# Optimization experiments

Measured on AMD Instinct MI355X. Metric: run time of the kernel, lower is better.

The kernel has to match this reference:

```python
import jax, jax.numpy as jnp
import numpy as np

BATCH, T, C = 32, 600, 64
DEPTH = 2            # logsig depth 2 -> [increments, Levy areas]
N_SEGMENTS = 50
N_HIDDENS = 512
LOGSIG_CH = C + C * (C - 1) // 2   # 2080, Lyndon-word count at depth 2
IN_SIZE = C + LOGSIG_CH            # 2144 = logsig + start point


def _t_vec(nT, n_segments):
    # matches: [int(round(x)) for x in np.linspace(1, nT, n_segments+1)]
    return np.asarray([int(round(v)) for v in np.linspace(1, nT, n_segments + 1)])


def setup_inputs() -> dict:
    key = jax.random.key(0)
    k0, k1, k2, k3, k4 = jax.random.split(key, 5)
    x = jax.random.normal(k0, (BATCH, T, C), jnp.float32)
    s = 1.0 / np.sqrt(N_HIDDENS)
    w_ih = jax.random.uniform(k1, (4 * N_HIDDENS, IN_SIZE), jnp.float32, -s, s)
    w_hh = jax.random.uniform(k2, (4 * N_HIDDENS, N_HIDDENS), jnp.float32, -s, s)
    b_ih = jax.random.uniform(k3, (4 * N_HIDDENS,), jnp.float32, -s, s)
    b_hh = jax.random.uniform(k4, (4 * N_HIDDENS,), jnp.float32, -s, s)
    return {"x": x, "w_ih": w_ih, "w_hh": w_hh, "b_ih": b_ih, "b_hh": b_hh}


def _logsig_and_start(x):
    """Depth-2 segmented log-signature + segment start points.
    Returns (logsig (B,S,LOGSIG_CH), start (B,S,C))."""
    B, nT, c = x.shape
    tv = _t_vec(nT, N_SEGMENTS)
    starts = tv[:-1] - 1               # segment start frame indices
    ends = tv[1:] - 1                  # segment end frame indices
    # step s (between frames s and s+1) belongs to segment i iff tv[i]-1 <= s < tv[i+1]-1
    step_ids = jnp.asarray(np.searchsorted(tv[1:] - 1, np.arange(nT - 1), side='right'))
    dx = x[:, 1:] - x[:, :-1]                            # (B, T-1, C)
    # per-step outer product x_{t-} (X) dx_t, then segmented sum over steps
    prod = jnp.einsum('btc,btd->btcd', x[:, :-1], dx)    # (B, T-1, C, C)
    Q = jax.ops.segment_sum(jnp.moveaxis(prod, 1, 0), step_ids,
                            num_segments=N_SEGMENTS)      # (S, B, C, C)
    xa = x[:, starts]                                    # (B, S, C)
    xb = x[:, ends]
    inc = xb - xa                                        # level-1 logsig
    # shift origin to segment start: P = sum (X_rel (X) dX)
    P = jnp.moveaxis(Q, 0, 1) - jnp.einsum('bsc,bsd->bscd', xa, inc)
    A = 0.5 * (P - jnp.swapaxes(P, -1, -2))              # Levy area (antisym)
    iu, ju = np.triu_indices(c, 1)                       # Lyndon words (i,j), i<j, lex order
    logsig = jnp.concatenate([inc, A[:, :, iu, ju]], axis=-1)
    return logsig, xa


def _lstm(feats, w_ih, w_hh, b_ih, b_hh):
    B = feats.shape[0]
    H = N_HIDDENS
    gx = jnp.einsum('bsf,gf->bsg', feats, w_ih) + b_ih + b_hh  # (B,S,4H)

    def step(carry, g_t):
        h, cc = carry
        g = g_t + h @ w_hh.T
        i, f, gg, o = jnp.split(g, 4, axis=-1)
        i = jax.nn.sigmoid(i); f = jax.nn.sigmoid(f)
        gg = jnp.tanh(gg); o = jax.nn.sigmoid(o)
        cc = f * cc + i * gg
        h = o * jnp.tanh(cc)
        return (h, cc), h

    h0 = jnp.zeros((B, H), feats.dtype)
    (_, _), hs = jax.lax.scan(step, (h0, h0), jnp.moveaxis(gx, 1, 0))
    return jnp.moveaxis(hs, 0, 1)                        # (B, S, H)


def reference(x, w_ih, w_hh, b_ih, b_hh):
    logsig, x_sp = _logsig_and_start(x)
    feats = jnp.concatenate([logsig, x_sp], axis=-1)      # (B, S, IN_SIZE)
    return _lstm(feats, w_ih, w_hh, b_ih, b_hh)
```

## Files before the change

kernel.cpp:

```cpp
#include <hip/hip_runtime.h>
#include <math.h>

typedef _Float16 f16;
typedef _Float16 f16x8 __attribute__((ext_vector_type(8)));
typedef _Float16 f16x4 __attribute__((ext_vector_type(4)));
typedef float    f32x4 __attribute__((ext_vector_type(4)));

#define BATCH 32
#define TT    600
#define CC    64
#define SEG   50
#define HH    512
#define G4    2048
#define FF    2144
#define MM    1600
#define MP    1664
#define NPAIR 2016
#define CVB   512
#define WRK   208
#define SLOT16 16384

struct TV { int v[51]; };

__device__ __forceinline__ void async_copy16(char* lds, const char* g) {
  __builtin_amdgcn_global_load_lds(
      (const __attribute__((address_space(1))) unsigned int*)g,
      (__attribute__((address_space(3))) unsigned int*)lds, 16, 0, 0);
}

__device__ __forceinline__ float sigm(float x) { return 1.f / (1.f + __expf(-x)); }
__device__ __forceinline__ float tanh_(float x) {
  float ax = fabsf(x);
  float e  = __expf(2.f * ax);
  float t  = 1.f - 2.f / (e + 1.f);
  return x < 0.f ? -t : t;
}
__device__ __forceinline__ unsigned short f16_bits(f16 v) {
  union { f16 f; unsigned short u; } c; c.f = v; return c.u;
}
__device__ __forceinline__ unsigned int f32_bits(float v) {
  union { float f; unsigned int u; } c; c.f = v; return c.u;
}

__global__ void prep_kernel(const float* __restrict__ x, f16* __restrict__ fhi, TV tv,
                            const float4* __restrict__ w_ih, const float4* __restrict__ w_hh,
                            f16x4* __restrict__ w16, f16x4* __restrict__ whh16,
                            unsigned int* __restrict__ ready) {
  __shared__ float xs[13 * CC];
  int m   = blockIdx.x;
  int tid = threadIdx.x;

  if (m >= MP) {
    int cb   = m - MP;
    int gtid = cb * 256 + tid;
    int nth  = CVB * 256;
    for (int i = gtid; i < G4 * FF / 4; i += nth) {
      float4 v = w_ih[i];
      f16x4 o = {(f16)v.x, (f16)v.y, (f16)v.z, (f16)v.w};
      w16[i] = o;
    }
    for (int i = gtid; i < G4 * HH / 4; i += nth) {
      float4 v = w_hh[i];
      f16x4 o = {(f16)v.x, (f16)v.y, (f16)v.z, (f16)v.w};
      whh16[i] = o;
    }
    if (cb == 0)
      for (int i = tid; i < 544; i += 256) ready[i] = 0u;
    return;
  }

  f16* rhi = fhi + (size_t)m * FF;
  if (m >= MM) {
    unsigned int* a = (unsigned int*)rhi;
    for (int i = tid; i < FF / 2; i += 256) a[i] = 0u;
    return;
  }
  int bb = m & 31, ss = m >> 5;
  int t0 = tv.v[ss] - 1, t1 = tv.v[ss + 1] - 1;
  int len = t1 - t0;
  for (int i = tid; i < (len + 1) * CC; i += 256)
    xs[i] = x[(size_t)bb * TT * CC + (size_t)(t0 + (i >> 6)) * CC + (i & 63)];
  __syncthreads();

  if (tid < CC) {
    float xa  = xs[tid];
    float inc = xs[len * CC + tid] - xa;
    rhi[tid] = (f16)inc;
    rhi[2080 + tid] = (f16)xa;
  }

  int p0 = tid * 8;
  if (p0 < NPAIR) {
    int c = 0, rem = p0;
    while (rem >= 63 - c) { rem -= 63 - c; c++; }
    int d = c + 1 + rem;
    int cs[8], dd[8];
#pragma unroll
    for (int i = 0; i < 8; i++) {
      cs[i] = c; dd[i] = d;
      d++; if (d == 64) { c++; d = c + 1; }
    }
    float acc[8], xc[8], xd[8];
#pragma unroll
    for (int i = 0; i < 8; i++) { acc[i] = 0.f; xc[i] = xs[cs[i]]; xd[i] = xs[dd[i]]; }
    for (int t = 1; t <= len; t++) {
#pragma unroll
      for (int i = 0; i < 8; i++) {
        float nc = xs[t * CC + cs[i]], nd = xs[t * CC + dd[i]];
        acc[i] += xc[i] * (nd - xd[i]) - xd[i] * (nc - xc[i]);
        xc[i] = nc; xd[i] = nd;
      }
    }
#pragma unroll
    for (int i = 0; i < 8; i++) {
      int ci = cs[i], di = dd[i];
      float xac = xs[ci], xad = xs[di];
      float incc = xs[len * CC + ci] - xac, incd = xs[len * CC + di] - xad;
      float v = 0.5f * acc[i] - 0.5f * (xac * incd - xad * incc);
      rhi[64 + p0 + i] = (f16)v;
    }
  }
}

__global__ __launch_bounds__(256) void fused_kernel(
    const f16* __restrict__ fhi, const f16* __restrict__ w16,
    const float* __restrict__ bih, const float* __restrict__ bhh,
    const f16* __restrict__ whh16, float* __restrict__ gx,
    unsigned short* __restrict__ hbuf, unsigned int* __restrict__ ready,
    unsigned int* __restrict__ gxcnt, float* __restrict__ out) {
  __shared__ __align__(16) char smem[40960];
  int tid  = threadIdx.x;
  int lane = tid & 63;

  if (blockIdx.x >= 32) {
    int w  = blockIdx.x - 32;
    int wn = tid >> 6;
    char* ldsA = smem;
    char* ldsB = smem + 4096;
    int rowq = tid >> 2;
    int colq = (tid & 3) * 8;
    int ldst = tid * 16;
    int quad16 = (lane >> 4) * 16;
    int am = lane & 15;
    unsigned int* gxa = (unsigned int*)gx;

    for (int t = 0; t < 2; t++) {
      int id = w + t * WRK;
      int mt = id >> 4, nt = id & 15;
      int m0 = mt * 64, n0 = nt * 128;

      const f16* pa  = fhi + (size_t)(m0 + rowq) * FF + colq;
      const f16* pb0 = w16 + (size_t)(n0 + rowq) * FF + colq;
      const f16* pb1 = pb0 + (size_t)64 * FF;

      f32x4 zero4 = {0.f, 0.f, 0.f, 0.f};
      f32x4 acc[4][2];
#pragma unroll
      for (int i = 0; i < 4; i++) { acc[i][0] = zero4; acc[i][1] = zero4; }

      for (int kt = 0; kt < FF / 32; kt++) {
        int koff = kt * 32;
        async_copy16(ldsA + ldst,        (const char*)(pa + koff));
        async_copy16(ldsB + ldst,        (const char*)(pb0 + koff));
        async_copy16(ldsB + 4096 + ldst, (const char*)(pb1 + koff));
        __syncthreads();

        f16x8 bfr[2];
#pragma unroll
        for (int ni = 0; ni < 2; ni++)
          bfr[ni] = *(const f16x8*)(ldsB + (wn * 32 + ni * 16 + am) * 64 + quad16);
#pragma unroll
        for (int mi = 0; mi < 4; mi++) {
          f16x8 ah = *(const f16x8*)(ldsA + (mi * 16 + am) * 64 + quad16);
#pragma unroll
          for (int ni = 0; ni < 2; ni++)
            acc[mi][ni] = __builtin_amdgcn_mfma_f32_16x16x32_f16(ah, bfr[ni], acc[mi][ni], 0, 0, 0);
        }
        __syncthreads();
      }

#pragma unroll
      for (int ni = 0; ni < 2; ni++) {
        int ncol = n0 + wn * 32 + ni * 16 + (lane & 15);
        float bv = bih[ncol] + bhh[ncol];
#pragma unroll
        for (int mi = 0; mi < 4; mi++) {
          int mrow = m0 + mi * 16 + (lane >> 4) * 4;
#pragma unroll
          for (int r = 0; r < 4; r++)
            __hip_atomic_store(gxa + (size_t)(mrow + r) * G4 + ncol,
                               f32_bits(acc[mi][ni][r] + bv),
                               __ATOMIC_RELAXED, __HIP_MEMORY_SCOPE_AGENT);
        }
      }
      __syncthreads();
      if (tid == 0)
        __hip_atomic_fetch_add(&gxcnt[mt], 1u, __ATOMIC_RELAXED,
                               __HIP_MEMORY_SCOPE_AGENT);
    }
    return;
  }

  f16* hs = (f16*)smem;
  float* gb = (float*)(smem + 32768);

  int gate = tid >> 6;
  int u0   = blockIdx.x * 16;
  int wg   = blockIdx.x;

  f16x8 bf[16];
  {
    const f16* wrow = whh16 + (size_t)(gate * HH + u0 + (lane & 15)) * HH + (lane >> 4) * 8;
#pragma unroll
    for (int ks = 0; ks < 16; ks++) bf[ks] = *(const f16x8*)(wrow + ks * 32);
  }

  int b1 = tid >> 4;
  int ul = tid & 15;
  float cst0 = 0.f, cst1 = 0.f;
  int aq  = (lane >> 4);
  int am  = (lane & 15);
  int col = lane & 15;
  int rbase = (lane >> 4) * 4;

  for (int s = 0; s < SEG; s++) {
    if ((s & 1) == 0) {
      if (tid == 0) {
        while (__hip_atomic_load(&gxcnt[s >> 1], __ATOMIC_RELAXED,
                                 __HIP_MEMORY_SCOPE_AGENT) < 16u)
          __builtin_amdgcn_s_sleep(1);
      }
      __syncthreads();
    }

    float gxr0[4], gxr1[4];
#pragma unroll
    for (int r = 0; r < 4; r++) {
      int b = rbase + r;
      gxr0[r] = gx[(size_t)((s << 5) + b) * G4 + gate * HH + u0 + col];
      gxr1[r] = gx[(size_t)((s << 5) + b + 16) * G4 + gate * HH + u0 + col];
    }

    f32x4 acc0 = {0.f, 0.f, 0.f, 0.f};
    f32x4 acc1 = {0.f, 0.f, 0.f, 0.f};

    if (s > 0) {
      unsigned int tgt = (unsigned int)s;
      if (tid < 32) {
        while (__hip_atomic_load(&ready[tid * 16], __ATOMIC_RELAXED,
                                 __HIP_MEMORY_SCOPE_AGENT) < tgt)
          __builtin_amdgcn_s_sleep(1);
      }
      __syncthreads();

      const char* hrd = (const char*)(hbuf + (size_t)s * SLOT16);
#pragma unroll
      for (int c = 0; c < 8; c++)
        async_copy16((char*)hs + c * 4096 + tid * 16, hrd + c * 4096 + tid * 16);
      __syncthreads();

#pragma unroll
      for (int ks = 0; ks < 16; ks++) {
        f16x8 a0 = *(const f16x8*)((char*)hs + (((ks * 4 + aq) * 32) + am) * 16);
        f16x8 a1 = *(const f16x8*)((char*)hs + (((ks * 4 + aq) * 32) + 16 + am) * 16);
        acc0 = __builtin_amdgcn_mfma_f32_16x16x32_f16(a0, bf[ks], acc0, 0, 0, 0);
        acc1 = __builtin_amdgcn_mfma_f32_16x16x32_f16(a1, bf[ks], acc1, 0, 0, 0);
      }
    }

#pragma unroll
    for (int r = 0; r < 4; r++) {
      int b = rbase + r;
      gb[(gate * 32 + b) * 16 + col]      = acc0[r] + gxr0[r];
      gb[(gate * 32 + b + 16) * 16 + col] = acc1[r] + gxr1[r];
    }
    __syncthreads();

    unsigned short* hwr = hbuf + (size_t)(s + 1) * SLOT16;
    int k = u0 + ul;
    float h0, h1;
    {
      float i_ = sigm(gb[(0 * 32 + b1) * 16 + ul]), f_ = sigm(gb[(1 * 32 + b1) * 16 + ul]);
      float g_ = tanh_(gb[(2 * 32 + b1) * 16 + ul]), o_ = sigm(gb[(3 * 32 + b1) * 16 + ul]);
      cst0 = f_ * cst0 + i_ * g_;
      h0 = o_ * tanh_(cst0);
      out[(size_t)(b1 * SEG + s) * HH + k] = h0;
    }
    {
      int b2 = b1 + 16;
      float i_ = sigm(gb[(0 * 32 + b2) * 16 + ul]), f_ = sigm(gb[(1 * 32 + b2) * 16 + ul]);
      float g_ = tanh_(gb[(2 * 32 + b2) * 16 + ul]), o_ = sigm(gb[(3 * 32 + b2) * 16 + ul]);
      cst1 = f_ * cst1 + i_ * g_;
      h1 = o_ * tanh_(cst1);
      out[(size_t)(b2 * SEG + s) * HH + k] = h1;
    }

    if (s < SEG - 1) {
      __hip_atomic_store(hwr + ((k >> 3) * 32 + b1) * 8 + (k & 7),
                         f16_bits((f16)h0), __ATOMIC_RELAXED, __HIP_MEMORY_SCOPE_AGENT);
      __hip_atomic_store(hwr + ((k >> 3) * 32 + (b1 + 16)) * 8 + (k & 7),
                         f16_bits((f16)h1), __ATOMIC_RELAXED, __HIP_MEMORY_SCOPE_AGENT);
      __syncthreads();
      if (tid == 0)
        __hip_atomic_store(&ready[wg * 16], (unsigned int)(s + 1),
                           __ATOMIC_RELAXED, __HIP_MEMORY_SCOPE_AGENT);
    }
  }
}

extern "C" void kernel_launch(void* const* d_in, const int* in_sizes, int n_in,
                              void* d_out, int out_size, void* d_ws, size_t ws_size,
                              hipStream_t stream) {
  const float* x    = (const float*)d_in[0];
  const float* w_ih = (const float*)d_in[1];
  const float* w_hh = (const float*)d_in[2];
  const float* b_ih = (const float*)d_in[3];
  const float* b_hh = (const float*)d_in[4];
  float* out = (float*)d_out;

  char* ws = (char*)d_ws;
  f16*   fhi   = (f16*)(ws + 0);
  f16*   w16   = (f16*)(ws + 7135232);
  f16*   whh16 = (f16*)(ws + 15921152);
  float* gx    = (float*)(ws + 18018304);
  unsigned short* hbuf  = (unsigned short*)(ws + 31649792);
  unsigned int*   ready = (unsigned int*)(ws + 33288192);

  TV tv;
  double step = 599.0 / 50.0;
  for (int i = 0; i <= 50; i++) {
    double v = (double)i * step + 1.0;
    tv.v[i] = (int)nearbyint(v);
  }
  tv.v[50] = 600;

  unsigned int* gxcnt = ready + 512;

  prep_kernel<<<dim3(MP + CVB), dim3(256), 0, stream>>>(
      x, fhi, tv, (const float4*)w_ih, (const float4*)w_hh,
      (f16x4*)w16, (f16x4*)whh16, ready);

  fused_kernel<<<dim3(32 + WRK), dim3(256), 0, stream>>>(
      fhi, w16, b_ih, b_hh, whh16, gx, hbuf, ready, gxcnt, out);
}
```

Baseline: 267.3 us.

## Replace per-step ready-flag barrier with sentinel-tagged hidden-state polling

The hidden-state buffer is pre-filled with an all-ones sentinel (0xFFFF in f16, a NaN pattern). The recurrent blocks then load their h fragments straight from global memory into registers and re-poll any 8-byte word whose top half still holds the sentinel. This drops the per-block ready counters, the spin on 32 flags, the LDS staging copy and two barriers on the serial critical path. Producers now stage h in LDS and publish it as 64-bit atomic stores. The risks are that correctness depends on a real h value never matching the sentinel, extra register pressure from the 64-entry array, and the cost of filling the whole buffer in prep.

```diff
diff --git a/kernel.cpp b/kernel.cpp
--- a/kernel.cpp
+++ b/kernel.cpp
@@ -35,9 +35,6 @@
   float t  = 1.f - 2.f / (e + 1.f);
   return x < 0.f ? -t : t;
 }
-__device__ __forceinline__ unsigned short f16_bits(f16 v) {
-  union { f16 f; unsigned short u; } c; c.f = v; return c.u;
-}
 __device__ __forceinline__ unsigned int f32_bits(float v) {
   union { float f; unsigned int u; } c; c.f = v; return c.u;
 }
@@ -45,7 +42,8 @@
 __global__ void prep_kernel(const float* __restrict__ x, f16* __restrict__ fhi, TV tv,
                             const float4* __restrict__ w_ih, const float4* __restrict__ w_hh,
                             f16x4* __restrict__ w16, f16x4* __restrict__ whh16,
-                            unsigned int* __restrict__ ready) {
+                            unsigned int* __restrict__ ready,
+                            unsigned int* __restrict__ hb32) {
   __shared__ float xs[13 * CC];
   int m   = blockIdx.x;
   int tid = threadIdx.x;
@@ -64,6 +62,7 @@
       f16x4 o = {(f16)v.x, (f16)v.y, (f16)v.z, (f16)v.w};
       whh16[i] = o;
     }
+    for (int i = gtid; i < SEG * SLOT16 / 2; i += nth) hb32[i] = 0xFFFFFFFFu;
     if (cb == 0)
       for (int i = tid; i < 544; i += 256) ready[i] = 0u;
     return;
@@ -128,7 +127,7 @@
     const f16* __restrict__ whh16, float* __restrict__ gx,
     unsigned short* __restrict__ hbuf, unsigned int* __restrict__ ready,
     unsigned int* __restrict__ gxcnt, float* __restrict__ out) {
-  __shared__ __align__(16) char smem[40960];
+  __shared__ __align__(16) char smem[12288];
   int tid  = threadIdx.x;
   int lane = tid & 63;
 
@@ -201,8 +200,8 @@
     return;
   }
 
-  f16* hs = (f16*)smem;
-  float* gb = (float*)(smem + 32768);
+  float* gb = (float*)smem;
+  f16* hstage = (f16*)(smem + 8192);
 
   int gate = tid >> 6;
   int u0   = blockIdx.x * 16;
@@ -222,6 +221,7 @@
   int am  = (lane & 15);
   int col = lane & 15;
   int rbase = (lane >> 4) * 4;
+  int cb0 = (aq * 32 + am) * 2;
 
   for (int s = 0; s < SEG; s++) {
     if ((s & 1) == 0) {
@@ -245,26 +245,36 @@
     f32x4 acc1 = {0.f, 0.f, 0.f, 0.f};
 
     if (s > 0) {
-      unsigned int tgt = (unsigned int)s;
-      if (tid < 32) {
-        while (__hip_atomic_load(&ready[tid * 16], __ATOMIC_RELAXED,
-                                 __HIP_MEMORY_SCOPE_AGENT) < tgt)
-          __builtin_amdgcn_s_sleep(1);
-      }
-      __syncthreads();
-
-      const char* hrd = (const char*)(hbuf + (size_t)s * SLOT16);
-#pragma unroll
-      for (int c = 0; c < 8; c++)
-        async_copy16((char*)hs + c * 4096 + tid * 16, hrd + c * 4096 + tid * 16);
-      __syncthreads();
-
+      const unsigned long long* hrd =
+          (const unsigned long long*)(hbuf + (size_t)s * SLOT16);
+      unsigned long long wq[64];
 #pragma unroll
       for (int ks = 0; ks < 16; ks++) {
-        f16x8 a0 = *(const f16x8*)((char*)hs + (((ks * 4 + aq) * 32) + am) * 16);
-        f16x8 a1 = *(const f16x8*)((char*)hs + (((ks * 4 + aq) * 32) + 16 + am) * 16);
-        acc0 = __builtin_amdgcn_mfma_f32_16x16x32_f16(a0, bf[ks], acc0, 0, 0, 0);
-        acc1 = __builtin_amdgcn_mfma_f32_16x16x32_f16(a1, bf[ks], acc1, 0, 0, 0);
+        int c0 = cb0 + ks * 256;
+        wq[ks * 4 + 0] = __hip_atomic_load(hrd + c0,      __ATOMIC_RELAXED, __HIP_MEMORY_SCOPE_AGENT);
+        wq[ks * 4 + 1] = __hip_atomic_load(hrd + c0 + 1,  __ATOMIC_RELAXED, __HIP_MEMORY_SCOPE_AGENT);
+        wq[ks * 4 + 2] = __hip_atomic_load(hrd + c0 + 32, __ATOMIC_RELAXED, __HIP_MEMORY_SCOPE_AGENT);
+        wq[ks * 4 + 3] = __hip_atomic_load(hrd + c0 + 33, __ATOMIC_RELAXED, __HIP_MEMORY_SCOPE_AGENT);
+      }
+      for (;;) {
+        bool pend = false;
+#pragma unroll
+        for (int i = 0; i < 64; i++) {
+          if ((unsigned)(wq[i] >> 48) == 0xFFFFu) {
+            pend = true;
+            int c = cb0 + (i >> 2) * 256 + ((i & 2) ? 32 : 0) + (i & 1);
+            wq[i] = __hip_atomic_load(hrd + c, __ATOMIC_RELAXED, __HIP_MEMORY_SCOPE_AGENT);
+          }
+        }
+        if (!pend) break;
+      }
+#pragma unroll
+      for (int ks = 0; ks < 16; ks++) {
+        union { unsigned long long q[2]; f16x8 v; } ua, ub;
+        ua.q[0] = wq[ks * 4 + 0]; ua.q[1] = wq[ks * 4 + 1];
+        ub.q[0] = wq[ks * 4 + 2]; ub.q[1] = wq[ks * 4 + 3];
+        acc0 = __builtin_amdgcn_mfma_f32_16x16x32_f16(ua.v, bf[ks], acc0, 0, 0, 0);
+        acc1 = __builtin_amdgcn_mfma_f32_16x16x32_f16(ub.v, bf[ks], acc1, 0, 0, 0);
       }
     }
 
@@ -276,7 +286,6 @@
     }
     __syncthreads();
 
-    unsigned short* hwr = hbuf + (size_t)(s + 1) * SLOT16;
     int k = u0 + ul;
     float h0, h1;
     {
@@ -296,14 +305,18 @@
     }
 
     if (s < SEG - 1) {
-      __hip_atomic_store(hwr + ((k >> 3) * 32 + b1) * 8 + (k & 7),
-                         f16_bits((f16)h0), __ATOMIC_RELAXED, __HIP_MEMORY_SCOPE_AGENT);
-      __hip_atomic_store(hwr + ((k >> 3) * 32 + (b1 + 16)) * 8 + (k & 7),
-                         f16_bits((f16)h1), __ATOMIC_RELAXED, __HIP_MEMORY_SCOPE_AGENT);
+      hstage[b1 * 20 + ul]        = (f16)h0;
+      hstage[(b1 + 16) * 20 + ul] = (f16)h1;
       __syncthreads();
-      if (tid == 0)
-        __hip_atomic_store(&ready[wg * 16], (unsigned int)(s + 1),
+      if (tid < 128) {
+        int kq = tid >> 5, b = tid & 31;
+        unsigned long long q = *(const unsigned long long*)(hstage + b * 20 + kq * 4);
+        unsigned long long* hw = (unsigned long long*)(hbuf + (size_t)(s + 1) * SLOT16);
+        __hip_atomic_store(hw + ((wg * 2 + (kq >> 1)) * 32 + b) * 2 + (kq & 1), q,
                            __ATOMIC_RELAXED, __HIP_MEMORY_SCOPE_AGENT);
+      }
+    } else {
+      __syncthreads();
     }
   }
 }
@@ -338,7 +351,7 @@
 
   prep_kernel<<<dim3(MP + CVB), dim3(256), 0, stream>>>(
       x, fhi, tv, (const float4*)w_ih, (const float4*)w_hh,
-      (f16x4*)w16, (f16x4*)whh16, ready);
+      (f16x4*)w16, (f16x4*)whh16, ready, (unsigned int*)hbuf);
 
   fused_kernel<<<dim3(32 + WRK), dim3(256), 0, stream>>>(
       fhi, w16, b_ih, b_hh, whh16, gx, hbuf, ready, gxcnt, out);
```

Result: slower. 391.3 us (+46.4%).

## Load h directly from global per wave and use per-wave readiness flags

Applied to the files above, without the earlier changes.

The recurrent step no longer stages the hidden state through LDS with async copies and two block barriers. Each wave now spins on its own readiness flags (64 flags, one per half-block) and loads its MFMA A-fragments straight from global memory. The h publish path packs f16 values through a small LDS stage into 64-bit atomic stores, issued by two waves that each signal their own flag after a vmcnt wait. Output stores move after the publish to keep them off the critical path, and LDS shrinks. The intent is to cut barrier and copy latency in the serial 50-step loop, at the cost of more polling traffic and more registers held in flight.

```diff
diff --git a/kernel.cpp b/kernel.cpp
--- a/kernel.cpp
+++ b/kernel.cpp
@@ -35,9 +35,6 @@
   float t  = 1.f - 2.f / (e + 1.f);
   return x < 0.f ? -t : t;
 }
-__device__ __forceinline__ unsigned short f16_bits(f16 v) {
-  union { f16 f; unsigned short u; } c; c.f = v; return c.u;
-}
 __device__ __forceinline__ unsigned int f32_bits(float v) {
   union { float f; unsigned int u; } c; c.f = v; return c.u;
 }
@@ -65,7 +62,7 @@
       whh16[i] = o;
     }
     if (cb == 0)
-      for (int i = tid; i < 544; i += 256) ready[i] = 0u;
+      for (int i = tid; i < 1056; i += 256) ready[i] = 0u;
     return;
   }
 
@@ -122,13 +119,13 @@
   }
 }
 
-__global__ __launch_bounds__(256) void fused_kernel(
+__global__ __launch_bounds__(256, 1) void fused_kernel(
     const f16* __restrict__ fhi, const f16* __restrict__ w16,
     const float* __restrict__ bih, const float* __restrict__ bhh,
     const f16* __restrict__ whh16, float* __restrict__ gx,
     unsigned short* __restrict__ hbuf, unsigned int* __restrict__ ready,
     unsigned int* __restrict__ gxcnt, float* __restrict__ out) {
-  __shared__ __align__(16) char smem[40960];
+  __shared__ __align__(16) char smem[12288];
   int tid  = threadIdx.x;
   int lane = tid & 63;
 
@@ -201,8 +198,8 @@
     return;
   }
 
-  f16* hs = (f16*)smem;
-  float* gb = (float*)(smem + 32768);
+  float* gb = (float*)smem;
+  f16* hstage = (f16*)(smem + 8192);
 
   int gate = tid >> 6;
   int u0   = blockIdx.x * 16;
@@ -216,21 +213,21 @@
   }
 
   int b1 = tid >> 4;
+  int b2 = b1 + 16;
   int ul = tid & 15;
   float cst0 = 0.f, cst1 = 0.f;
   int aq  = (lane >> 4);
   int am  = (lane & 15);
   int col = lane & 15;
   int rbase = (lane >> 4) * 4;
+  int k = u0 + ul;
 
   for (int s = 0; s < SEG; s++) {
     if ((s & 1) == 0) {
-      if (tid == 0) {
-        while (__hip_atomic_load(&gxcnt[s >> 1], __ATOMIC_RELAXED,
-                                 __HIP_MEMORY_SCOPE_AGENT) < 16u)
-          __builtin_amdgcn_s_sleep(1);
-      }
-      __syncthreads();
+      while (__hip_atomic_load(&gxcnt[s >> 1], __ATOMIC_RELAXED,
+                               __HIP_MEMORY_SCOPE_AGENT) < 16u)
+        __builtin_amdgcn_s_sleep(2);
+      asm volatile("" ::: "memory");
     }
 
     float gxr0[4], gxr1[4];
@@ -246,25 +243,23 @@
 
     if (s > 0) {
       unsigned int tgt = (unsigned int)s;
-      if (tid < 32) {
-        while (__hip_atomic_load(&ready[tid * 16], __ATOMIC_RELAXED,
-                                 __HIP_MEMORY_SCOPE_AGENT) < tgt)
-          __builtin_amdgcn_s_sleep(1);
-      }
-      __syncthreads();
-
-      const char* hrd = (const char*)(hbuf + (size_t)s * SLOT16);
-#pragma unroll
-      for (int c = 0; c < 8; c++)
-        async_copy16((char*)hs + c * 4096 + tid * 16, hrd + c * 4096 + tid * 16);
-      __syncthreads();
-
+      while (__hip_atomic_load(&ready[lane * 16], __ATOMIC_RELAXED,
+                               __HIP_MEMORY_SCOPE_AGENT) < tgt)
+        __builtin_amdgcn_s_sleep(1);
+      asm volatile("" ::: "memory");
+
+      const char* hrd = (const char*)(hbuf + (size_t)s * SLOT16)
+                      + (size_t)(aq * 32 + am) * 16;
+      f16x8 a0[16], a1[16];
 #pragma unroll
       for (int ks = 0; ks < 16; ks++) {
-        f16x8 a0 = *(const f16x8*)((char*)hs + (((ks * 4 + aq) * 32) + am) * 16);
-        f16x8 a1 = *(const f16x8*)((char*)hs + (((ks * 4 + aq) * 32) + 16 + am) * 16);
-        acc0 = __builtin_amdgcn_mfma_f32_16x16x32_f16(a0, bf[ks], acc0, 0, 0, 0);
-        acc1 = __builtin_amdgcn_mfma_f32_16x16x32_f16(a1, bf[ks], acc1, 0, 0, 0);
+        a0[ks] = *(const f16x8*)(hrd + ks * 2048);
+        a1[ks] = *(const f16x8*)(hrd + ks * 2048 + 256);
+      }
+#pragma unroll
+      for (int ks = 0; ks < 16; ks++) {
+        acc0 = __builtin_amdgcn_mfma_f32_16x16x32_f16(a0[ks], bf[ks], acc0, 0, 0, 0);
+        acc1 = __builtin_amdgcn_mfma_f32_16x16x32_f16(a1[ks], bf[ks], acc1, 0, 0, 0);
       }
     }
 
@@ -276,35 +271,40 @@
     }
     __syncthreads();
 
-    unsigned short* hwr = hbuf + (size_t)(s + 1) * SLOT16;
-    int k = u0 + ul;
     float h0, h1;
     {
       float i_ = sigm(gb[(0 * 32 + b1) * 16 + ul]), f_ = sigm(gb[(1 * 32 + b1) * 16 + ul]);
       float g_ = tanh_(gb[(2 * 32 + b1) * 16 + ul]), o_ = sigm(gb[(3 * 32 + b1) * 16 + ul]);
       cst0 = f_ * cst0 + i_ * g_;
       h0 = o_ * tanh_(cst0);
-      out[(size_t)(b1 * SEG + s) * HH + k] = h0;
     }
     {
-      int b2 = b1 + 16;
       float i_ = sigm(gb[(0 * 32 + b2) * 16 + ul]), f_ = sigm(gb[(1 * 32 + b2) * 16 + ul]);
       float g_ = tanh_(gb[(2 * 32 + b2) * 16 + ul]), o_ = sigm(gb[(3 * 32 + b2) * 16 + ul]);
       cst1 = f_ * cst1 + i_ * g_;
       h1 = o_ * tanh_(cst1);
-      out[(size_t)(b2 * SEG + s) * HH + k] = h1;
     }
 
     if (s < SEG - 1) {
-      __hip_atomic_store(hwr + ((k >> 3) * 32 + b1) * 8 + (k & 7),
-                         f16_bits((f16)h0), __ATOMIC_RELAXED, __HIP_MEMORY_SCOPE_AGENT);
-      __hip_atomic_store(hwr + ((k >> 3) * 32 + (b1 + 16)) * 8 + (k & 7),
-                         f16_bits((f16)h1), __ATOMIC_RELAXED, __HIP_MEMORY_SCOPE_AGENT);
-      __syncthreads();
-      if (tid == 0)
-        __hip_atomic_store(&ready[wg * 16], (unsigned int)(s + 1),
+      hstage[b1 * 20 + ul] = (f16)h0;
+      hstage[b2 * 20 + ul] = (f16)h1;
+    }
+    __syncthreads();
+
+    if (s < SEG - 1 && tid < 128) {
+      int kq = tid >> 5, b = tid & 31;
+      unsigned long long q = *(const unsigned long long*)(hstage + b * 20 + kq * 4);
+      unsigned long long* hw = (unsigned long long*)(hbuf + (size_t)(s + 1) * SLOT16);
+      __hip_atomic_store(hw + ((wg * 2 + (kq >> 1)) * 32 + b) * 2 + (kq & 1), q,
+                         __ATOMIC_RELAXED, __HIP_MEMORY_SCOPE_AGENT);
+      asm volatile("s_waitcnt vmcnt(0)" ::: "memory");
+      if ((tid & 63) == 0)
+        __hip_atomic_store(&ready[(wg * 2 + (tid >> 6)) * 16], (unsigned int)(s + 1),
                            __ATOMIC_RELAXED, __HIP_MEMORY_SCOPE_AGENT);
     }
+
+    out[(size_t)(b1 * SEG + s) * HH + k] = h0;
+    out[(size_t)(b2 * SEG + s) * HH + k] = h1;
   }
 }
 
@@ -334,7 +334,7 @@
   }
   tv.v[50] = 600;
 
-  unsigned int* gxcnt = ready + 512;
+  unsigned int* gxcnt = ready + 1024;
 
   prep_kernel<<<dim3(MP + CVB), dim3(256), 0, stream>>>(
       x, fhi, tv, (const float4*)w_ih, (const float4*)w_hh,
```

After: 382.1 us. 42.9% more time.

## Multi-buffer the gx GEMM K-loop with deep async prefetch; defer LSTM output stores

Applied to the files above, without the earlier changes.

The input-projection GEMM K-loop moves from a single LDS buffer with two barriers per step to a 5-slot ring that keeps three K-tiles of async global-to-LDS loads in flight. It uses explicit vmcnt waits and one barrier per iteration. This aims to hide global load latency behind MFMA work, at the cost of more shared memory, which may lower occupancy. Separately, the recurrent loop now writes the h outputs after publishing the ready flag, so those global stores are off the critical cross-workgroup dependency path.

```diff
diff --git a/kernel.cpp b/kernel.cpp
--- a/kernel.cpp
+++ b/kernel.cpp
@@ -19,6 +19,8 @@
 #define CVB   512
 #define WRK   208
 #define SLOT16 16384
+#define KT    67
+#define BUFB  12288
 
 struct TV { int v[51]; };
 
@@ -128,15 +130,13 @@
     const f16* __restrict__ whh16, float* __restrict__ gx,
     unsigned short* __restrict__ hbuf, unsigned int* __restrict__ ready,
     unsigned int* __restrict__ gxcnt, float* __restrict__ out) {
-  __shared__ __align__(16) char smem[40960];
+  __shared__ __align__(16) char smem[61440];
   int tid  = threadIdx.x;
   int lane = tid & 63;
 
   if (blockIdx.x >= 32) {
     int w  = blockIdx.x - 32;
     int wn = tid >> 6;
-    char* ldsA = smem;
-    char* ldsB = smem + 4096;
     int rowq = tid >> 2;
     int colq = (tid & 3) * 8;
     int ldst = tid * 16;
@@ -158,13 +158,35 @@
 #pragma unroll
       for (int i = 0; i < 4; i++) { acc[i][0] = zero4; acc[i][1] = zero4; }
 
-      for (int kt = 0; kt < FF / 32; kt++) {
-        int koff = kt * 32;
-        async_copy16(ldsA + ldst,        (const char*)(pa + koff));
-        async_copy16(ldsB + ldst,        (const char*)(pb0 + koff));
-        async_copy16(ldsB + 4096 + ldst, (const char*)(pb1 + koff));
-        __syncthreads();
-
+      for (int kp = 0; kp < 3; kp++) {
+        char* b = smem + kp * BUFB;
+        int koff = kp * 32;
+        async_copy16(b + ldst,        (const char*)(pa + koff));
+        async_copy16(b + 4096 + ldst, (const char*)(pb0 + koff));
+        async_copy16(b + 8192 + ldst, (const char*)(pb1 + koff));
+      }
+
+      for (int kt = 0; kt < KT; kt++) {
+        if (kt + 3 < KT) {
+          char* b = smem + ((kt + 3) % 5) * BUFB;
+          int koff = (kt + 3) * 32;
+          async_copy16(b + ldst,        (const char*)(pa + koff));
+          async_copy16(b + 4096 + ldst, (const char*)(pb0 + koff));
+          async_copy16(b + 8192 + ldst, (const char*)(pb1 + koff));
+          asm volatile("s_waitcnt vmcnt(9)" ::: "memory");
+        } else if (kt + 3 == KT) {
+          asm volatile("s_waitcnt vmcnt(6)" ::: "memory");
+        } else if (kt + 2 == KT) {
+          asm volatile("s_waitcnt vmcnt(3)" ::: "memory");
+        } else {
+          asm volatile("s_waitcnt vmcnt(0)" ::: "memory");
+        }
+        __builtin_amdgcn_s_barrier();
+        __builtin_amdgcn_sched_barrier(0);
+
+        char* bb   = smem + (kt % 5) * BUFB;
+        char* ldsA = bb;
+        char* ldsB = bb + 4096;
         f16x8 bfr[2];
 #pragma unroll
         for (int ni = 0; ni < 2; ni++)
@@ -176,7 +198,6 @@
           for (int ni = 0; ni < 2; ni++)
             acc[mi][ni] = __builtin_amdgcn_mfma_f32_16x16x32_f16(ah, bfr[ni], acc[mi][ni], 0, 0, 0);
         }
-        __syncthreads();
       }
 
 #pragma unroll
@@ -284,7 +305,6 @@
       float g_ = tanh_(gb[(2 * 32 + b1) * 16 + ul]), o_ = sigm(gb[(3 * 32 + b1) * 16 + ul]);
       cst0 = f_ * cst0 + i_ * g_;
       h0 = o_ * tanh_(cst0);
-      out[(size_t)(b1 * SEG + s) * HH + k] = h0;
     }
     {
       int b2 = b1 + 16;
@@ -292,7 +312,6 @@
       float g_ = tanh_(gb[(2 * 32 + b2) * 16 + ul]), o_ = sigm(gb[(3 * 32 + b2) * 16 + ul]);
       cst1 = f_ * cst1 + i_ * g_;
       h1 = o_ * tanh_(cst1);
-      out[(size_t)(b2 * SEG + s) * HH + k] = h1;
     }
 
     if (s < SEG - 1) {
@@ -305,6 +324,9 @@
         __hip_atomic_store(&ready[wg * 16], (unsigned int)(s + 1),
                            __ATOMIC_RELAXED, __HIP_MEMORY_SCOPE_AGENT);
     }
+
+    out[(size_t)(b1 * SEG + s) * HH + k] = h0;
+    out[(size_t)((b1 + 16) * SEG + s) * HH + k] = h1;
   }
 }
 
```

New measurement: 245.1 us. -8.3%, faster.
